# Kernel tuning notes

Measured on AMD Instinct MI355X. Metric: run time of the kernel, lower is better.

The kernel has to match this reference:

```python
import jax, jax.numpy as jnp
import numpy as np

B, S, HIDDEN = 4, 2048, 1024
NUM_EXPERTS = 8
TOP_K = 4
EPS = 1e-6


def setup_inputs() -> dict:
    key = jax.random.key(0)
    k0, k1, k2 = jax.random.split(key, 3)
    x = jax.random.normal(k0, (B, S, HIDDEN), dtype=jnp.float32)
    Wg = jax.random.normal(k1, (HIDDEN, NUM_EXPERTS), dtype=jnp.float32) * 0.02
    bg = jnp.zeros((NUM_EXPERTS,), dtype=jnp.float32)
    W = jax.random.normal(k2, (NUM_EXPERTS, HIDDEN, HIDDEN), dtype=jnp.float32) * 0.02
    b = jnp.zeros((NUM_EXPERTS, HIDDEN), dtype=jnp.float32)
    return {"x": x, "Wg": Wg, "bg": bg, "W": W, "b": b}


def reference(x, Wg, bg, W, b):
    Bb, Ss, D = x.shape
    xf = x.reshape(-1, D)                       # [T, D]
    T = xf.shape[0]

    # --- router ---
    router_logits = xf @ Wg + bg                # [T, E]
    router_probs = jax.nn.softmax(router_logits, axis=-1)
    top_k_probs, top_k_indices = jax.lax.top_k(router_probs, TOP_K)  # [T, K]
    top_k_weights = top_k_probs / (top_k_probs.sum(axis=-1, keepdims=True) + EPS)
    expert_mask = jax.nn.one_hot(top_k_indices, NUM_EXPERTS, dtype=jnp.float32).sum(axis=1)  # [T, E]

    # --- experts: original computes every expert on every token then masks;
    # same math expressed as one batched GEMM + gather ---
    all_out = jnp.einsum('td,edf->etf', xf, W) + b[:, None, :]  # [E, T, D]
    sel = all_out[top_k_indices.T, jnp.arange(T)[None, :]]      # [K, T, D]
    moe_output = jnp.einsum('tk,ktd->td', top_k_weights, sel).reshape(Bb, Ss, D)

    # --- load-balancing aux loss ---
    aux_loss = jnp.dot(expert_mask.mean(axis=0), router_probs.mean(axis=0)) * NUM_EXPERTS
    return moe_output, aux_loss
```

## Files before the change

### kernel.cpp

```cpp
#include <hip/hip_runtime.h>
#include <hip/hip_bf16.h>

#define T_TOK 8192
#define DH    1024
#define NE    8
#define TK    4

typedef unsigned short u16;
typedef __bf16 bf16x8 __attribute__((ext_vector_type(8)));
typedef float  f32x4  __attribute__((ext_vector_type(4)));

__device__ __forceinline__ u16 f2b(float f) {
    union { float f; unsigned u; } v; v.f = f;
    unsigned u = v.u;
    u += 0x7FFFu + ((u >> 16) & 1u);
    return (u16)(u >> 16);
}
__device__ __forceinline__ float b2f(u16 h) {
    union { unsigned u; float f; } v; v.u = ((unsigned)h) << 16;
    return v.f;
}
__device__ __forceinline__ void glds16(const u16* g, u16* l) {
    __builtin_amdgcn_global_load_lds((const __attribute__((address_space(1))) void*)g,
                                     (__attribute__((address_space(3))) void*)l, 16, 0, 0);
}

#define FENCE() asm volatile("" ::: "memory")
#define SBAR()  do { FENCE(); __builtin_amdgcn_s_barrier(); FENCE(); } while (0)
#define WAITLGKM0() do { asm volatile("s_waitcnt lgkmcnt(0)" ::: "memory"); \
                         __builtin_amdgcn_sched_barrier(0); } while (0)

__global__ __launch_bounds__(256) void cast_w_kernel(const float* __restrict__ W,
                                                     u16* __restrict__ wbt) {
    __shared__ float tile[64][65];
    const int e  = blockIdx.z;
    const int d0 = blockIdx.y * 64;
    const int f0 = blockIdx.x * 64;
    const int r  = threadIdx.x >> 4;
    const int c4 = (threadIdx.x & 15) * 4;
    const float* src = W + ((size_t)e << 20) + (size_t)d0 * DH + f0;
    #pragma unroll
    for (int i = 0; i < 4; i++) {
        const int row = i * 16 + r;
        const float4 v = *(const float4*)(src + (size_t)row * DH + c4);
        tile[row][c4]     = v.x;
        tile[row][c4 + 1] = v.y;
        tile[row][c4 + 2] = v.z;
        tile[row][c4 + 3] = v.w;
    }
    __syncthreads();
    u16* dst = wbt + ((size_t)e << 20) + (size_t)f0 * DH + d0;
    #pragma unroll
    for (int i = 0; i < 4; i++) {
        const int orow = i * 16 + r;
        ushort4 o;
        o.x = f2b(tile[c4][orow]);
        o.y = f2b(tile[c4 + 1][orow]);
        o.z = f2b(tile[c4 + 2][orow]);
        o.w = f2b(tile[c4 + 3][orow]);
        *(ushort4*)(dst + (size_t)orow * DH + c4) = o;
    }
}

__global__ __launch_bounds__(512) void router_kernel(
    const float* __restrict__ x, const float* __restrict__ Wg, const float* __restrict__ bg,
    u16* __restrict__ xb,
    int* __restrict__ bucket_tok, float* __restrict__ bucket_w,
    int* __restrict__ tk_e, float* __restrict__ tk_w,
    int* __restrict__ cnt, float* __restrict__ probsum)
{
    __shared__ int   lcnt[NE];
    __shared__ float lprob[NE];
    __shared__ int   gbase[NE];
    const int tid = threadIdx.x;
    const int wv = tid >> 6, lane = tid & 63;
    const int t = blockIdx.x * 8 + wv;
    if (tid < NE) { lcnt[tid] = 0; lprob[tid] = 0.f; }
    __syncthreads();

    float a[NE] = {};
    {
        const float* xr = x + (size_t)t * DH;
        u16* xbr = xb + (size_t)t * DH;
        #pragma unroll
        for (int it = 0; it < 4; it++) {
            const int d = it * 256 + lane * 4;
            const float4 v = *(const float4*)(xr + d);
            ushort4 o;
            o.x = f2b(v.x); o.y = f2b(v.y); o.z = f2b(v.z); o.w = f2b(v.w);
            *(ushort4*)(xbr + d) = o;
            const float* wr = Wg + d * NE;
            #pragma unroll
            for (int e = 0; e < NE; e++)
                a[e] += v.x * wr[e] + v.y * wr[NE + e] + v.z * wr[2 * NE + e] + v.w * wr[3 * NE + e];
        }
    }
    #pragma unroll
    for (int e = 0; e < NE; e++) {
        float v = a[e];
        #pragma unroll
        for (int off = 32; off > 0; off >>= 1) v += __shfl_down(v, off);
        a[e] = v;
    }

    int idx4[TK]; float w4[TK]; int off4[TK];
    if (lane == 0) {
        float logits[NE], probs[NE];
        float mx = -1e30f;
        #pragma unroll
        for (int e = 0; e < NE; e++) { logits[e] = a[e] + bg[e]; mx = fmaxf(mx, logits[e]); }
        float Z = 0.f;
        #pragma unroll
        for (int e = 0; e < NE; e++) { probs[e] = expf(logits[e] - mx); Z += probs[e]; }
        const float rZ = 1.f / Z;
        #pragma unroll
        for (int e = 0; e < NE; e++) probs[e] *= rZ;

        float rem2[NE];
        #pragma unroll
        for (int e = 0; e < NE; e++) rem2[e] = probs[e];
        float s4 = 0.f;
        #pragma unroll
        for (int k = 0; k < TK; k++) {
            int best = 0; float bv = rem2[0];
            #pragma unroll
            for (int e = 1; e < NE; e++) if (rem2[e] > bv) { bv = rem2[e]; best = e; }
            idx4[k] = best; w4[k] = bv; s4 += bv; rem2[best] = -1e30f;
        }
        const float rs = 1.f / (s4 + 1e-6f);
        #pragma unroll
        for (int k = 0; k < TK; k++) {
            w4[k] *= rs;
            tk_e[t * TK + k] = idx4[k];
            tk_w[t * TK + k] = w4[k];
            off4[k] = atomicAdd(&lcnt[idx4[k]], 1);
        }
        #pragma unroll
        for (int e = 0; e < NE; e++) atomicAdd(&lprob[e], probs[e]);
    }
    __syncthreads();
    if (tid < NE) {
        gbase[tid] = atomicAdd(&cnt[tid], lcnt[tid]);
        atomicAdd(&probsum[tid], lprob[tid]);
    }
    __syncthreads();
    if (lane == 0) {
        #pragma unroll
        for (int k = 0; k < TK; k++) {
            const int e = idx4[k];
            const int slot = gbase[e] + off4[k];
            bucket_tok[e * T_TOK + slot] = (t << 2) | k;
            bucket_w[e * T_TOK + slot]   = w4[k];
        }
    }
}

__global__ __launch_bounds__(512, 2) void moe_gemm_kernel(
    const u16* __restrict__ xb, const u16* __restrict__ wbt,
    const int* __restrict__ bucket_tok, const float* __restrict__ bucket_w,
    const int* __restrict__ cnt, u16* __restrict__ y)
{
    __shared__ u16 As[2][256 * 64];
    __shared__ u16 Bs[2][256 * 64];
    __shared__ int   s_tok[256];
    __shared__ float s_w[256];

    const int tid  = threadIdx.x;
    const int lane = tid & 63;
    const int wid  = tid >> 6;
    const int wr   = wid >> 2;
    const int wc   = wid & 3;
    const int fr   = lane & 15;
    const int fq   = (lane >> 4) * 8;
    const int swz  = (fr & 7) << 3;
    const int gsw  = ((lane & 7) ^ (lane >> 3)) * 8;
    const int crow = lane >> 3;

    for (int vt = blockIdx.x; vt < 1024; vt += 256) {
        const int mb = vt >> 5;
        const int e  = (vt >> 2) & 7;
        const int nb = vt & 3;
        const int M  = cnt[e];
        const int m0 = mb << 8;
        if (m0 >= M) continue;
        const int n0 = nb << 8;

        __syncthreads();
        if (tid < 256) {
            const int slot = m0 + tid;
            if (slot < M) {
                s_tok[tid] = bucket_tok[e * T_TOK + slot];
                s_w[tid]   = bucket_w[e * T_TOK + slot];
            } else { s_tok[tid] = -1; s_w[tid] = 0.f; }
        }
        __syncthreads();

        const u16* gA[4]; const u16* gB[4];
        #pragma unroll
        for (int q = 0; q < 4; q++) {
            const int row = wid * 32 + q * 8 + crow;
            const int tok = s_tok[row];
            gA[q] = xb + (size_t)(tok >= 0 ? (tok >> 2) : 0) * DH + gsw;
            gB[q] = wbt + ((size_t)e << 20) + (size_t)(n0 + row) * DH + gsw;
        }

        f32x4 acc[8][4] = {};

        auto STAGE = [&](int kt) {
            const int p  = kt & 1;
            const int ko = kt * 64;
            #pragma unroll
            for (int q = 0; q < 4; q++)
                glds16(gA[q] + ko, &As[p][(wid * 4 + q) * 512]);
            #pragma unroll
            for (int q = 0; q < 4; q++)
                glds16(gB[q] + ko, &Bs[p][(wid * 4 + q) * 512]);
        };

        STAGE(0); STAGE(1);
        asm volatile("s_waitcnt vmcnt(8)" ::: "memory");
        SBAR();

        const int arow = (wr * 128 + fr) * 64;
        const int brow = (wc * 64  + fr) * 64;
        const int c0 = fq ^ swz;
        const int c1 = (32 + fq) ^ swz;

        bf16x8 afL[4][2], afH[4][2], bfL[2][2], bfH[2][2];

        for (int kt = 0; kt < 16; ++kt) {
            const int p = kt & 1;
            const u16* Ap = &As[p][0];
            const u16* Bp = &Bs[p][0];

            #pragma unroll
            for (int mi = 0; mi < 4; mi++) {
                afL[mi][0] = *(const bf16x8*)&Ap[arow + mi * 1024 + c0];
                afL[mi][1] = *(const bf16x8*)&Ap[arow + mi * 1024 + c1];
            }
            #pragma unroll
            for (int nj = 0; nj < 2; nj++) {
                bfL[nj][0] = *(const bf16x8*)&Bp[brow + nj * 1024 + c0];
                bfL[nj][1] = *(const bf16x8*)&Bp[brow + nj * 1024 + c1];
            }
            SBAR(); WAITLGKM0();
            __builtin_amdgcn_s_setprio(1);
            #pragma unroll
            for (int mi = 0; mi < 4; mi++)
                #pragma unroll
                for (int nj = 0; nj < 2; nj++) {
                    acc[mi][nj] = __builtin_amdgcn_mfma_f32_16x16x32_bf16(afL[mi][0], bfL[nj][0], acc[mi][nj], 0, 0, 0);
                    acc[mi][nj] = __builtin_amdgcn_mfma_f32_16x16x32_bf16(afL[mi][1], bfL[nj][1], acc[mi][nj], 0, 0, 0);
                }
            __builtin_amdgcn_s_setprio(0);
            SBAR();

            #pragma unroll
            for (int nj = 0; nj < 2; nj++) {
                bfH[nj][0] = *(const bf16x8*)&Bp[brow + (nj + 2) * 1024 + c0];
                bfH[nj][1] = *(const bf16x8*)&Bp[brow + (nj + 2) * 1024 + c1];
            }
            SBAR(); WAITLGKM0();
            __builtin_amdgcn_s_setprio(1);
            #pragma unroll
            for (int mi = 0; mi < 4; mi++)
                #pragma unroll
                for (int nj = 0; nj < 2; nj++) {
                    acc[mi][nj + 2] = __builtin_amdgcn_mfma_f32_16x16x32_bf16(afL[mi][0], bfH[nj][0], acc[mi][nj + 2], 0, 0, 0);
                    acc[mi][nj + 2] = __builtin_amdgcn_mfma_f32_16x16x32_bf16(afL[mi][1], bfH[nj][1], acc[mi][nj + 2], 0, 0, 0);
                }
            __builtin_amdgcn_s_setprio(0);
            SBAR();

            #pragma unroll
            for (int mi = 0; mi < 4; mi++) {
                afH[mi][0] = *(const bf16x8*)&Ap[arow + (mi + 4) * 1024 + c0];
                afH[mi][1] = *(const bf16x8*)&Ap[arow + (mi + 4) * 1024 + c1];
            }
            SBAR(); WAITLGKM0();
            __builtin_amdgcn_s_setprio(1);
            #pragma unroll
            for (int mi = 0; mi < 4; mi++)
                #pragma unroll
                for (int nj = 0; nj < 2; nj++) {
                    acc[mi + 4][nj + 2] = __builtin_amdgcn_mfma_f32_16x16x32_bf16(afH[mi][0], bfH[nj][0], acc[mi + 4][nj + 2], 0, 0, 0);
                    acc[mi + 4][nj + 2] = __builtin_amdgcn_mfma_f32_16x16x32_bf16(afH[mi][1], bfH[nj][1], acc[mi + 4][nj + 2], 0, 0, 0);
                }
            __builtin_amdgcn_s_setprio(0);
            SBAR();

            if (kt < 14) STAGE(kt + 2);
            __builtin_amdgcn_s_setprio(1);
            #pragma unroll
            for (int mi = 0; mi < 4; mi++)
                #pragma unroll
                for (int nj = 0; nj < 2; nj++) {
                    acc[mi + 4][nj] = __builtin_amdgcn_mfma_f32_16x16x32_bf16(afH[mi][0], bfL[nj][0], acc[mi + 4][nj], 0, 0, 0);
                    acc[mi + 4][nj] = __builtin_amdgcn_mfma_f32_16x16x32_bf16(afH[mi][1], bfL[nj][1], acc[mi + 4][nj], 0, 0, 0);
                }
            __builtin_amdgcn_s_setprio(0);
            if (kt < 14)       asm volatile("s_waitcnt vmcnt(8)" ::: "memory");
            else if (kt == 14) asm volatile("s_waitcnt vmcnt(0)" ::: "memory");
            SBAR();
        }

        const int cl = lane & 15;
        const int rb = (lane >> 4) * 4;
        #pragma unroll
        for (int mi = 0; mi < 8; mi++) {
            #pragma unroll
            for (int r = 0; r < 4; r++) {
                const int srow = wr * 128 + mi * 16 + rb + r;
                const int tok = s_tok[srow];
                if (tok < 0) continue;
                const float w = s_w[srow];
                u16* yr = y + (size_t)tok * DH + (n0 + wc * 64 + cl);
                #pragma unroll
                for (int nj = 0; nj < 4; nj++)
                    yr[nj * 16] = f2b(acc[mi][nj][r] * w);
            }
        }
    }
}

__global__ __launch_bounds__(256) void combine_kernel(
    const u16* __restrict__ y, const int* __restrict__ tk_e, const float* __restrict__ tk_w,
    const float* __restrict__ bexp,
    const int* __restrict__ cnt, const float* __restrict__ probsum,
    float* __restrict__ out, float* __restrict__ out_aux)
{
    const int t = blockIdx.x;
    const int c = threadIdx.x * 4;
    if (t == 0 && threadIdx.x == 0) {
        float s = 0.f;
        for (int e = 0; e < NE; e++) s += (float)cnt[e] * probsum[e];
        out_aux[0] = s * (float)NE / ((float)T_TOK * (float)T_TOK);
    }
    float o0 = 0.f, o1 = 0.f, o2 = 0.f, o3 = 0.f;
    #pragma unroll
    for (int k = 0; k < TK; k++) {
        const int e   = tk_e[t * TK + k];
        const float w = tk_w[t * TK + k];
        const ushort4 yv = *(const ushort4*)(y + ((size_t)(t * TK + k)) * DH + c);
        const float4  bv = *(const float4*)(bexp + (size_t)e * DH + c);
        o0 += b2f(yv.x) + w * bv.x;
        o1 += b2f(yv.y) + w * bv.y;
        o2 += b2f(yv.z) + w * bv.z;
        o3 += b2f(yv.w) + w * bv.w;
    }
    float4 ov = {o0, o1, o2, o3};
    *(float4*)(out + (size_t)t * DH + c) = ov;
}

extern "C" void kernel_launch(void* const* d_in, const int* in_sizes, int n_in,
                              void* d_out, int out_size, void* d_ws, size_t ws_size,
                              hipStream_t stream)
{
    const float* x  = (const float*)d_in[0];
    const float* Wg = (const float*)d_in[1];
    const float* bg = (const float*)d_in[2];
    const float* W  = (const float*)d_in[3];
    const float* b  = (const float*)d_in[4];
    float* out = (float*)d_out;

    char* ws = (char*)d_ws;
    u16*   xb         = (u16*)(ws);
    u16*   wbt        = (u16*)(ws + 16777216);
    u16*   y          = (u16*)(ws + 33554432);
    int*   bucket_tok = (int*)(ws + 100663296);
    float* bucket_w   = (float*)(ws + 100925440);
    int*   tk_e       = (int*)(ws + 101187584);
    float* tk_w       = (float*)(ws + 101318656);
    int*   cnt        = (int*)(ws + 101449728);
    float* probsum    = (float*)(ws + 101449760);

    hipMemsetAsync(cnt, 0, 64, stream);

    cast_w_kernel<<<dim3(16, 16, NE), 256, 0, stream>>>(W, wbt);
    router_kernel<<<1024, 512, 0, stream>>>(x, Wg, bg, xb, bucket_tok, bucket_w, tk_e, tk_w, cnt, probsum);
    moe_gemm_kernel<<<dim3(256), 512, 0, stream>>>(xb, wbt, bucket_tok, bucket_w, cnt, y);
    combine_kernel<<<8192, 256, 0, stream>>>(y, tk_e, tk_w, b, cnt, probsum, out, out + (size_t)T_TOK * DH);
}
```

Before: 267.3 us.

## Fuse weight cast with router and retile MoE GEMM to 128x256 triple-buffered

Merges the weight cast and router kernels into one launch, using block-index ranges to split the work, which saves one launch and lets both phases overlap. The router now reads the gate weights as float4 vectors. The expert GEMM tile shrinks from 256x256 to 128x256 and gets a three-stage LDS pipeline with split loads for the A, low-B and high-B parts. Blocks are assigned to fixed experts with a strided tile schedule, and launch bounds move to one block per CU. Smaller tiles reduce wasted rows on partial expert buckets but lower data reuse per tile, and the new wait counts are delicate.

```diff
diff --git a/kernel.cpp b/kernel.cpp
--- a/kernel.cpp
+++ b/kernel.cpp
@@ -29,52 +29,56 @@
 #define SBAR()  do { FENCE(); __builtin_amdgcn_s_barrier(); FENCE(); } while (0)
 #define WAITLGKM0() do { asm volatile("s_waitcnt lgkmcnt(0)" ::: "memory"); \
                          __builtin_amdgcn_sched_barrier(0); } while (0)
-
-__global__ __launch_bounds__(256) void cast_w_kernel(const float* __restrict__ W,
-                                                     u16* __restrict__ wbt) {
-    __shared__ float tile[64][65];
-    const int e  = blockIdx.z;
-    const int d0 = blockIdx.y * 64;
-    const int f0 = blockIdx.x * 64;
-    const int r  = threadIdx.x >> 4;
-    const int c4 = (threadIdx.x & 15) * 4;
-    const float* src = W + ((size_t)e << 20) + (size_t)d0 * DH + f0;
-    #pragma unroll
-    for (int i = 0; i < 4; i++) {
-        const int row = i * 16 + r;
-        const float4 v = *(const float4*)(src + (size_t)row * DH + c4);
-        tile[row][c4]     = v.x;
-        tile[row][c4 + 1] = v.y;
-        tile[row][c4 + 2] = v.z;
-        tile[row][c4 + 3] = v.w;
-    }
-    __syncthreads();
-    u16* dst = wbt + ((size_t)e << 20) + (size_t)f0 * DH + d0;
-    #pragma unroll
-    for (int i = 0; i < 4; i++) {
-        const int orow = i * 16 + r;
-        ushort4 o;
-        o.x = f2b(tile[c4][orow]);
-        o.y = f2b(tile[c4 + 1][orow]);
-        o.z = f2b(tile[c4 + 2][orow]);
-        o.w = f2b(tile[c4 + 3][orow]);
-        *(ushort4*)(dst + (size_t)orow * DH + c4) = o;
-    }
-}
-
-__global__ __launch_bounds__(512) void router_kernel(
+#define WAITVM(n) asm volatile("s_waitcnt vmcnt(" #n ")" ::: "memory")
+
+__global__ __launch_bounds__(256) void prep_kernel(
+    const float* __restrict__ W, u16* __restrict__ wbt,
     const float* __restrict__ x, const float* __restrict__ Wg, const float* __restrict__ bg,
     u16* __restrict__ xb,
     int* __restrict__ bucket_tok, float* __restrict__ bucket_w,
     int* __restrict__ tk_e, float* __restrict__ tk_w,
     int* __restrict__ cnt, float* __restrict__ probsum)
 {
+    __shared__ float tile[64][65];
     __shared__ int   lcnt[NE];
     __shared__ float lprob[NE];
     __shared__ int   gbase[NE];
+
+    if (blockIdx.x < 2048) {
+        const unsigned u = blockIdx.x;
+        const int f0 = (u & 15) * 64;
+        const int d0 = ((u >> 4) & 15) * 64;
+        const int e  = u >> 8;
+        const int r  = threadIdx.x >> 4;
+        const int c4 = (threadIdx.x & 15) * 4;
+        const float* src = W + ((size_t)e << 20) + (size_t)d0 * DH + f0;
+        #pragma unroll
+        for (int i = 0; i < 4; i++) {
+            const int row = i * 16 + r;
+            const float4 v = *(const float4*)(src + (size_t)row * DH + c4);
+            tile[row][c4]     = v.x;
+            tile[row][c4 + 1] = v.y;
+            tile[row][c4 + 2] = v.z;
+            tile[row][c4 + 3] = v.w;
+        }
+        __syncthreads();
+        u16* dst = wbt + ((size_t)e << 20) + (size_t)f0 * DH + d0;
+        #pragma unroll
+        for (int i = 0; i < 4; i++) {
+            const int orow = i * 16 + r;
+            ushort4 o;
+            o.x = f2b(tile[c4][orow]);
+            o.y = f2b(tile[c4 + 1][orow]);
+            o.z = f2b(tile[c4 + 2][orow]);
+            o.w = f2b(tile[c4 + 3][orow]);
+            *(ushort4*)(dst + (size_t)orow * DH + c4) = o;
+        }
+        return;
+    }
+
     const int tid = threadIdx.x;
     const int wv = tid >> 6, lane = tid & 63;
-    const int t = blockIdx.x * 8 + wv;
+    const int t = (blockIdx.x - 2048) * 4 + wv;
     if (tid < NE) { lcnt[tid] = 0; lprob[tid] = 0.f; }
     __syncthreads();
 
@@ -82,6 +86,7 @@
     {
         const float* xr = x + (size_t)t * DH;
         u16* xbr = xb + (size_t)t * DH;
+        const float4* wg = (const float4*)Wg;
         #pragma unroll
         for (int it = 0; it < 4; it++) {
             const int d = it * 256 + lane * 4;
@@ -89,10 +94,18 @@
             ushort4 o;
             o.x = f2b(v.x); o.y = f2b(v.y); o.z = f2b(v.z); o.w = f2b(v.w);
             *(ushort4*)(xbr + d) = o;
-            const float* wr = Wg + d * NE;
-            #pragma unroll
-            for (int e = 0; e < NE; e++)
-                a[e] += v.x * wr[e] + v.y * wr[NE + e] + v.z * wr[2 * NE + e] + v.w * wr[3 * NE + e];
+            const float4 w0l = wg[2 * (d + 0)], w0h = wg[2 * (d + 0) + 1];
+            const float4 w1l = wg[2 * (d + 1)], w1h = wg[2 * (d + 1) + 1];
+            const float4 w2l = wg[2 * (d + 2)], w2h = wg[2 * (d + 2) + 1];
+            const float4 w3l = wg[2 * (d + 3)], w3h = wg[2 * (d + 3) + 1];
+            a[0] += v.x * w0l.x + v.y * w1l.x + v.z * w2l.x + v.w * w3l.x;
+            a[1] += v.x * w0l.y + v.y * w1l.y + v.z * w2l.y + v.w * w3l.y;
+            a[2] += v.x * w0l.z + v.y * w1l.z + v.z * w2l.z + v.w * w3l.z;
+            a[3] += v.x * w0l.w + v.y * w1l.w + v.z * w2l.w + v.w * w3l.w;
+            a[4] += v.x * w0h.x + v.y * w1h.x + v.z * w2h.x + v.w * w3h.x;
+            a[5] += v.x * w0h.y + v.y * w1h.y + v.z * w2h.y + v.w * w3h.y;
+            a[6] += v.x * w0h.z + v.y * w1h.z + v.z * w2h.z + v.w * w3h.z;
+            a[7] += v.x * w0h.w + v.y * w1h.w + v.z * w2h.w + v.w * w3h.w;
         }
     }
     #pragma unroll
@@ -155,15 +168,15 @@
     }
 }
 
-__global__ __launch_bounds__(512, 2) void moe_gemm_kernel(
+__global__ __launch_bounds__(512, 1) void moe_gemm_kernel(
     const u16* __restrict__ xb, const u16* __restrict__ wbt,
     const int* __restrict__ bucket_tok, const float* __restrict__ bucket_w,
     const int* __restrict__ cnt, u16* __restrict__ y)
 {
-    __shared__ u16 As[2][256 * 64];
-    __shared__ u16 Bs[2][256 * 64];
-    __shared__ int   s_tok[256];
-    __shared__ float s_w[256];
+    __shared__ u16 As[3][128 * 64];
+    __shared__ u16 Bs[3][256 * 64];
+    __shared__ int   s_tok[128];
+    __shared__ float s_w[128];
 
     const int tid  = threadIdx.x;
     const int lane = tid & 63;
@@ -176,17 +189,25 @@
     const int gsw  = ((lane & 7) ^ (lane >> 3)) * 8;
     const int crow = lane >> 3;
 
-    for (int vt = blockIdx.x; vt < 1024; vt += 256) {
-        const int mb = vt >> 5;
-        const int e  = (vt >> 2) & 7;
-        const int nb = vt & 3;
-        const int M  = cnt[e];
-        const int m0 = mb << 8;
+    const int i0  = 2 * wid, i1 = 2 * wid + 1;
+    const int blC0 = (i0 >> 2) * 8 + (i0 & 3);
+    const int blC1 = (i1 >> 2) * 8 + (i1 & 3);
+    const int bhC0 = blC0 + 4, bhC1 = blC1 + 4;
+
+    const int e  = blockIdx.x & 7;
+    const int cc = blockIdx.x >> 3;
+    const int M  = cnt[e];
+
+    for (int j = 0; j < 8; ++j) {
+        const int idx = j * 32 + cc;
+        const int mb = idx >> 2;
+        const int nb = idx & 3;
+        const int m0 = mb << 7;
         if (m0 >= M) continue;
         const int n0 = nb << 8;
 
         __syncthreads();
-        if (tid < 256) {
+        if (tid < 128) {
             const int slot = m0 + tid;
             if (slot < M) {
                 s_tok[tid] = bucket_tok[e * T_TOK + slot];
@@ -195,122 +216,99 @@
         }
         __syncthreads();
 
-        const u16* gA[4]; const u16* gB[4];
-        #pragma unroll
-        for (int q = 0; q < 4; q++) {
-            const int row = wid * 32 + q * 8 + crow;
-            const int tok = s_tok[row];
-            gA[q] = xb + (size_t)(tok >= 0 ? (tok >> 2) : 0) * DH + gsw;
-            gB[q] = wbt + ((size_t)e << 20) + (size_t)(n0 + row) * DH + gsw;
-        }
-
-        f32x4 acc[8][4] = {};
-
-        auto STAGE = [&](int kt) {
-            const int p  = kt & 1;
-            const int ko = kt * 64;
-            #pragma unroll
-            for (int q = 0; q < 4; q++)
-                glds16(gA[q] + ko, &As[p][(wid * 4 + q) * 512]);
-            #pragma unroll
-            for (int q = 0; q < 4; q++)
-                glds16(gB[q] + ko, &Bs[p][(wid * 4 + q) * 512]);
-        };
-
-        STAGE(0); STAGE(1);
-        asm volatile("s_waitcnt vmcnt(8)" ::: "memory");
+        const int rA0 = i0 * 8 + crow, rA1 = i1 * 8 + crow;
+        const int tA0 = s_tok[rA0], tA1 = s_tok[rA1];
+        const u16* gA0 = xb + (size_t)(tA0 >= 0 ? (tA0 >> 2) : 0) * DH + gsw;
+        const u16* gA1 = xb + (size_t)(tA1 >= 0 ? (tA1 >> 2) : 0) * DH + gsw;
+        const u16* wbe = wbt + ((size_t)e << 20);
+        const u16* gBL0 = wbe + (size_t)(n0 + blC0 * 8 + crow) * DH + gsw;
+        const u16* gBL1 = wbe + (size_t)(n0 + blC1 * 8 + crow) * DH + gsw;
+        const u16* gBH0 = wbe + (size_t)(n0 + bhC0 * 8 + crow) * DH + gsw;
+        const u16* gBH1 = wbe + (size_t)(n0 + bhC1 * 8 + crow) * DH + gsw;
+
+        f32x4 acc[4][4] = {};
+
+        #define STG_A(kt)  do { glds16(gA0  + (kt) * 64, &As[(kt) % 3][i0   * 512]); \
+                                glds16(gA1  + (kt) * 64, &As[(kt) % 3][i1   * 512]); } while (0)
+        #define STG_BL(kt) do { glds16(gBL0 + (kt) * 64, &Bs[(kt) % 3][blC0 * 512]); \
+                                glds16(gBL1 + (kt) * 64, &Bs[(kt) % 3][blC1 * 512]); } while (0)
+        #define STG_BH(kt) do { glds16(gBH0 + (kt) * 64, &Bs[(kt) % 3][bhC0 * 512]); \
+                                glds16(gBH1 + (kt) * 64, &Bs[(kt) % 3][bhC1 * 512]); } while (0)
+
+        STG_A(0); STG_BL(0); STG_BH(0); STG_A(1); STG_BL(1); STG_BH(1); STG_A(2); STG_BL(2);
+        WAITVM(12);
         SBAR();
 
-        const int arow = (wr * 128 + fr) * 64;
-        const int brow = (wc * 64  + fr) * 64;
+        const int arow = (wr * 64 + fr) * 64;
+        const int brow = (wc * 64 + fr) * 64;
         const int c0 = fq ^ swz;
         const int c1 = (32 + fq) ^ swz;
 
-        bf16x8 afL[4][2], afH[4][2], bfL[2][2], bfH[2][2];
-
+        #pragma unroll
         for (int kt = 0; kt < 16; ++kt) {
-            const int p = kt & 1;
-            const u16* Ap = &As[p][0];
-            const u16* Bp = &Bs[p][0];
+            const u16* Ap = &As[kt % 3][0];
+            const u16* Bp = &Bs[kt % 3][0];
+            bf16x8 af[4][2], bl[2][2], bh[2][2];
 
             #pragma unroll
             for (int mi = 0; mi < 4; mi++) {
-                afL[mi][0] = *(const bf16x8*)&Ap[arow + mi * 1024 + c0];
-                afL[mi][1] = *(const bf16x8*)&Ap[arow + mi * 1024 + c1];
+                af[mi][0] = *(const bf16x8*)&Ap[arow + mi * 1024 + c0];
+                af[mi][1] = *(const bf16x8*)&Ap[arow + mi * 1024 + c1];
             }
             #pragma unroll
             for (int nj = 0; nj < 2; nj++) {
-                bfL[nj][0] = *(const bf16x8*)&Bp[brow + nj * 1024 + c0];
-                bfL[nj][1] = *(const bf16x8*)&Bp[brow + nj * 1024 + c1];
+                bl[nj][0] = *(const bf16x8*)&Bp[brow + nj * 1024 + c0];
+                bl[nj][1] = *(const bf16x8*)&Bp[brow + nj * 1024 + c1];
             }
+            if (kt <= 13) STG_BH(kt + 2);
+            asm volatile("s_waitcnt lgkmcnt(8)" ::: "memory");
             SBAR(); WAITLGKM0();
             __builtin_amdgcn_s_setprio(1);
             #pragma unroll
             for (int mi = 0; mi < 4; mi++)
                 #pragma unroll
                 for (int nj = 0; nj < 2; nj++) {
-                    acc[mi][nj] = __builtin_amdgcn_mfma_f32_16x16x32_bf16(afL[mi][0], bfL[nj][0], acc[mi][nj], 0, 0, 0);
-                    acc[mi][nj] = __builtin_amdgcn_mfma_f32_16x16x32_bf16(afL[mi][1], bfL[nj][1], acc[mi][nj], 0, 0, 0);
+                    acc[mi][nj] = __builtin_amdgcn_mfma_f32_16x16x32_bf16(af[mi][0], bl[nj][0], acc[mi][nj], 0, 0, 0);
+                    acc[mi][nj] = __builtin_amdgcn_mfma_f32_16x16x32_bf16(af[mi][1], bl[nj][1], acc[mi][nj], 0, 0, 0);
                 }
             __builtin_amdgcn_s_setprio(0);
+            if (kt <= 13)      WAITVM(12);
+            else if (kt == 14) WAITVM(6);
+            else               WAITVM(0);
             SBAR();
 
             #pragma unroll
             for (int nj = 0; nj < 2; nj++) {
-                bfH[nj][0] = *(const bf16x8*)&Bp[brow + (nj + 2) * 1024 + c0];
-                bfH[nj][1] = *(const bf16x8*)&Bp[brow + (nj + 2) * 1024 + c1];
+                bh[nj][0] = *(const bf16x8*)&Bp[brow + (nj + 2) * 1024 + c0];
+                bh[nj][1] = *(const bf16x8*)&Bp[brow + (nj + 2) * 1024 + c1];
             }
+            if (kt <= 12) { STG_A(kt + 3); STG_BL(kt + 3); }
             SBAR(); WAITLGKM0();
             __builtin_amdgcn_s_setprio(1);
             #pragma unroll
             for (int mi = 0; mi < 4; mi++)
                 #pragma unroll
                 for (int nj = 0; nj < 2; nj++) {
-                    acc[mi][nj + 2] = __builtin_amdgcn_mfma_f32_16x16x32_bf16(afL[mi][0], bfH[nj][0], acc[mi][nj + 2], 0, 0, 0);
-                    acc[mi][nj + 2] = __builtin_amdgcn_mfma_f32_16x16x32_bf16(afL[mi][1], bfH[nj][1], acc[mi][nj + 2], 0, 0, 0);
+                    acc[mi][nj + 2] = __builtin_amdgcn_mfma_f32_16x16x32_bf16(af[mi][0], bh[nj][0], acc[mi][nj + 2], 0, 0, 0);
+                    acc[mi][nj + 2] = __builtin_amdgcn_mfma_f32_16x16x32_bf16(af[mi][1], bh[nj][1], acc[mi][nj + 2], 0, 0, 0);
                 }
             __builtin_amdgcn_s_setprio(0);
+            if (kt <= 12)      WAITVM(12);
+            else if (kt == 13) WAITVM(8);
+            else if (kt == 14) WAITVM(2);
             SBAR();
-
-            #pragma unroll
-            for (int mi = 0; mi < 4; mi++) {
-                afH[mi][0] = *(const bf16x8*)&Ap[arow + (mi + 4) * 1024 + c0];
-                afH[mi][1] = *(const bf16x8*)&Ap[arow + (mi + 4) * 1024 + c1];
-            }
-            SBAR(); WAITLGKM0();
-            __builtin_amdgcn_s_setprio(1);
-            #pragma unroll
-            for (int mi = 0; mi < 4; mi++)
-                #pragma unroll
-                for (int nj = 0; nj < 2; nj++) {
-                    acc[mi + 4][nj + 2] = __builtin_amdgcn_mfma_f32_16x16x32_bf16(afH[mi][0], bfH[nj][0], acc[mi + 4][nj + 2], 0, 0, 0);
-                    acc[mi + 4][nj + 2] = __builtin_amdgcn_mfma_f32_16x16x32_bf16(afH[mi][1], bfH[nj][1], acc[mi + 4][nj + 2], 0, 0, 0);
-                }
-            __builtin_amdgcn_s_setprio(0);
-            SBAR();
-
-            if (kt < 14) STAGE(kt + 2);
-            __builtin_amdgcn_s_setprio(1);
-            #pragma unroll
-            for (int mi = 0; mi < 4; mi++)
-                #pragma unroll
-                for (int nj = 0; nj < 2; nj++) {
-                    acc[mi + 4][nj] = __builtin_amdgcn_mfma_f32_16x16x32_bf16(afH[mi][0], bfL[nj][0], acc[mi + 4][nj], 0, 0, 0);
-                    acc[mi + 4][nj] = __builtin_amdgcn_mfma_f32_16x16x32_bf16(afH[mi][1], bfL[nj][1], acc[mi + 4][nj], 0, 0, 0);
-                }
-            __builtin_amdgcn_s_setprio(0);
-            if (kt < 14)       asm volatile("s_waitcnt vmcnt(8)" ::: "memory");
-            else if (kt == 14) asm volatile("s_waitcnt vmcnt(0)" ::: "memory");
-            SBAR();
-        }
+        }
+        #undef STG_A
+        #undef STG_BL
+        #undef STG_BH
 
         const int cl = lane & 15;
         const int rb = (lane >> 4) * 4;
         #pragma unroll
-        for (int mi = 0; mi < 8; mi++) {
+        for (int mi = 0; mi < 4; mi++) {
             #pragma unroll
             for (int r = 0; r < 4; r++) {
-                const int srow = wr * 128 + mi * 16 + rb + r;
+                const int srow = wr * 64 + mi * 16 + rb + r;
                 const int tok = s_tok[srow];
                 if (tok < 0) continue;
                 const float w = s_w[srow];
@@ -376,8 +374,8 @@
 
     hipMemsetAsync(cnt, 0, 64, stream);
 
-    cast_w_kernel<<<dim3(16, 16, NE), 256, 0, stream>>>(W, wbt);
-    router_kernel<<<1024, 512, 0, stream>>>(x, Wg, bg, xb, bucket_tok, bucket_w, tk_e, tk_w, cnt, probsum);
+    prep_kernel<<<4096, 256, 0, stream>>>(W, wbt, x, Wg, bg, xb,
+                                          bucket_tok, bucket_w, tk_e, tk_w, cnt, probsum);
     moe_gemm_kernel<<<dim3(256), 512, 0, stream>>>(xb, wbt, bucket_tok, bucket_w, cnt, y);
     combine_kernel<<<8192, 256, 0, stream>>>(y, tk_e, tk_w, b, cnt, probsum, out, out + (size_t)T_TOK * DH);
 }
```

Result: slower. 310.7 us (+16.3%).
